# Performance work log

Hardware: AMD Instinct MI355X
Metric: run time of the kernel (lower is better)

Reference implementation:

```python
import jax, jax.numpy as jnp
import numpy as np

B, T, N_DYN, D_H, D_Z, HID = 256, 1024, 20, 64, 128, 64


def setup_inputs() -> dict:
    key = jax.random.key(0)
    ks = jax.random.split(key, 12)

    def uinit(k, shape):
        lim = 1.0 / np.sqrt(shape[0])
        return jax.random.uniform(k, shape, jnp.float32, -lim, lim)

    return dict(
        z0=jax.random.normal(ks[0], (B, D_Z), jnp.float32),
        # non-decreasing event times per sample (hours)
        t_dyn=jnp.cumsum(jax.random.uniform(ks[1], (B, T), jnp.float32), axis=1),
        Y_dyn=jax.random.normal(ks[2], (B, T, N_DYN), jnp.float32),
        M_dyn=jax.random.uniform(ks[3], (B, T, N_DYN), jnp.float32),
        H_dyn=jax.random.normal(ks[4], (B, T, D_H), jnp.float32),  # h_path.query(t_k) per step
        dyn_lens=jax.random.randint(ks[5], (B,), 0, T),
        ode_W0=uinit(ks[6], (D_Z, HID)), ode_b0=jnp.zeros((HID,), jnp.float32),
        ode_W1=uinit(ks[7], (HID, HID)), ode_b1=jnp.zeros((HID,), jnp.float32),
        ode_W2=uinit(ks[8], (HID, D_Z)), ode_b2=jnp.zeros((D_Z,), jnp.float32),
        W_ih=uinit(ks[9], (2 * N_DYN + D_H, 3 * D_Z)), b_ih=jnp.zeros((3 * D_Z,), jnp.float32),
        W_hh=uinit(ks[10], (D_Z, 3 * D_Z)), b_hh=jnp.zeros((3 * D_Z,), jnp.float32),
    )


def reference(z0, t_dyn, Y_dyn, M_dyn, H_dyn, dyn_lens,
              ode_W0, ode_b0, ode_W1, ode_b1, ode_W2, ode_b2,
              W_ih, b_ih, W_hh, b_hh):
    def ode_f(z):
        h = jnp.tanh(z @ ode_W0 + ode_b0)
        h = jnp.tanh(h @ ode_W1 + ode_b1)
        return h @ ode_W2 + ode_b2

    def evolve(z, dt):  # dt: (B,1); single-step RK4 of dz/ds = f(z)*dt over s in [0,1]
        f = lambda z_: ode_f(z_) * dt
        k1 = f(z)
        k2 = f(z + 0.5 * k1)
        k3 = f(z + 0.5 * k2)
        k4 = f(z + k3)
        return z + (k1 + 2.0 * k2 + 2.0 * k3 + k4) / 6.0

    def gru(x, h):  # torch GRUCell math
        gi = x @ W_ih + b_ih
        gh = h @ W_hh + b_hh
        i_r, i_u, i_n = jnp.split(gi, 3, axis=-1)
        h_r, h_u, h_n = jnp.split(gh, 3, axis=-1)
        r = jax.nn.sigmoid(i_r + h_r)
        u = jax.nn.sigmoid(i_u + h_u)
        n = jnp.tanh(i_n + r * h_n)
        return (1.0 - u) * n + u * h

    def step(carry, xs):
        z, t_prev = carry
        t_k, y_k, m_k, h_k, k = xs
        dt = jnp.clip(t_k - t_prev, 0.0)[:, None]
        # at k==0 dt is exactly 0 so evolve(z,0)==z, matching the torch k==0 branch
        z_ode = evolve(z, dt)
        inp = jnp.concatenate([y_k, m_k, h_k], axis=-1)  # (B, 2*n_dyn + d_h)
        z_new = gru(inp, z_ode)
        active = (k < dyn_lens).astype(z.dtype)[:, None]
        z = z_new * active + z_ode * (1.0 - active)
        return (z, t_k), z

    Tm = t_dyn.shape[1]
    xs = (t_dyn.T,
          jnp.transpose(Y_dyn, (1, 0, 2)),
          jnp.transpose(M_dyn, (1, 0, 2)),
          jnp.transpose(H_dyn, (1, 0, 2)),
          jnp.arange(Tm))
    (z_final, _), Z = jax.lax.scan(step, (z0, t_dyn[:, 0]), xs)
    return z_final, jnp.transpose(Z, (1, 0, 2))  # (B,d_z), (B,T,d_z)
```

## Files before the change

### kernel.cpp

```cpp
#include <hip/hip_runtime.h>
#include <cstdint>
#include <cstddef>

#define B_    256
#define T_    1024
#define NDYN  20
#define DH    64
#define DZ    128
#define HIDN  64
#define GCOLS 384
#define XDIM  104

#define WHH_LDS_G 25
#define WHH_REG   28

__device__ __forceinline__ int cpad(int k) { return (k >> 4) * 20 + (k & 15); }

template<int CTRL, int XORMASK>
__device__ __forceinline__ float dpp_sum(float v) {
#if __has_builtin(__builtin_amdgcn_mov_dpp)
  int o = __builtin_amdgcn_mov_dpp(__float_as_int(v), CTRL, 0xF, 0xF, true);
  return v + __int_as_float(o);
#else
  return v + __shfl_xor(v, XORMASK);
#endif
}

__device__ __forceinline__ float tanh_fast(float x) {
  float a = __expf(-2.f * fabsf(x));
  return copysignf((1.f - a) / (1.f + a), x);
}
__device__ __forceinline__ float sigm(float x) { return 1.f / (1.f + __expf(-x)); }

__global__ __launch_bounds__(384, 1) void odernn_kernel(
    const float* __restrict__ z0, const float* __restrict__ tdyn,
    const float* __restrict__ Y, const float* __restrict__ Mm,
    const float* __restrict__ Hh, const int* __restrict__ lens,
    const float* __restrict__ W0, const float* __restrict__ b0,
    const float* __restrict__ W1, const float* __restrict__ b1,
    const float* __restrict__ W2, const float* __restrict__ b2,
    const float* __restrict__ Wih, const float* __restrict__ bih,
    const float* __restrict__ Whh, const float* __restrict__ bhh,
    const float* __restrict__ gi_pre, float* __restrict__ out, int use_gi)
{
  const int tid = threadIdx.x;
  const int b   = blockIdx.x;

  __shared__ __align__(16) float vinP[160];
  __shared__ __align__(16) float h1P[80];
  __shared__ __align__(16) float h2P[80];
  __shared__ __align__(16) float zodeL[128];
  __shared__ float zcurL[128];
  __shared__ float gateL[384];
  __shared__ float gateN[128];
  __shared__ float xsL[112];
  __shared__ __align__(16) float4 WhhP4[WHH_LDS_G * 384];

  float wA[32], wB[32], whh28[WHH_REG];

  #pragma unroll 1
  for (int g = 0; g < WHH_LDS_G; ++g) {
    float4 w;
    w.x = Whh[(4 * g + 0) * GCOLS + tid];
    w.y = Whh[(4 * g + 1) * GCOLS + tid];
    w.z = Whh[(4 * g + 2) * GCOLS + tid];
    w.w = Whh[(4 * g + 3) * GCOLS + tid];
    WhhP4[g * 384 + tid] = w;
  }
  #pragma unroll
  for (int i = 0; i < WHH_REG; ++i)
    whh28[i] = Whh[(4 * WHH_LDS_G + i) * GCOLS + tid];

  if (tid < 256) {
    const int jg = tid >> 3, p = tid & 7, j0 = 2 * jg, kb = 16 * p;
    #pragma unroll
    for (int i = 0; i < 16; ++i) {
      wA[i]      = W0[(kb + i) * HIDN + j0];
      wA[16 + i] = W0[(kb + i) * HIDN + j0 + 1];
    }
  } else {
    const int u = tid - 128, jg = u >> 2, p = u & 3, j0 = 2 * jg, kb = 16 * p;
    #pragma unroll
    for (int i = 0; i < 16; ++i) {
      wA[i]      = W2[(kb + i) * DZ + j0];
      wA[16 + i] = W2[(kb + i) * DZ + j0 + 1];
    }
  }
  if (tid < 128) {
    const int jg = tid >> 2, p = tid & 3, j0 = 2 * jg, kb = 16 * p;
    #pragma unroll
    for (int i = 0; i < 16; ++i) {
      wB[i]      = W1[(kb + i) * HIDN + j0];
      wB[16 + i] = W1[(kb + i) * HIDN + j0 + 1];
    }
  } else if (tid < 256) {
    const int u = tid - 128, jg = u >> 2, p = u & 3, j0 = 2 * jg, kb = 16 * p;
    #pragma unroll
    for (int i = 0; i < 16; ++i) {
      wB[i]      = W2[(kb + i) * DZ + j0];
      wB[16 + i] = W2[(kb + i) * DZ + j0 + 1];
    }
  }

  float b0r = 0.f, b1r = 0.f, b2r = 0.f;
  if (tid < 256 && (tid & 7) < 2) b0r = b0[2 * (tid >> 3) + (tid & 7)];
  if (tid < 128 && (tid & 3) < 2) b1r = b1[2 * (tid >> 2) + (tid & 3)];
  if (tid >= 128 && ((tid - 128) & 3) < 2)
    b2r = b2[2 * ((tid - 128) >> 2) + ((tid - 128) & 3)];
  const float bhhr = bhh[tid];
  const float bihr = bih[tid];
  const int   lenb = lens[b];

  if (tid < 128) {
    float zv = z0[(size_t)b * DZ + tid];
    vinP[cpad(tid)] = zv;
    zcurL[tid] = zv;
  }
  __syncthreads();

  float* Zbase = out + (size_t)B_ * DZ;
  const float* tdb = tdyn + (size_t)b * T_;

  const int u2 = tid - 128, jg2 = u2 >> 2, p2 = u2 & 3;
  const int j2 = 2 * jg2 + p2;

  #pragma unroll 1
  for (int t = 0; t < T_; ++t) {
    const size_t bt = (size_t)b * T_ + t;
    const float dt = (t == 0) ? 0.f : fmaxf(tdb[t] - tdb[t - 1], 0.f);

    float gival = 0.f;
    if (use_gi) {
      gival = gi_pre[bt * GCOLS + tid];
    } else if (tid < XDIM) {
      float v;
      if (tid < 20)      v = Y[bt * NDYN + tid];
      else if (tid < 40) v = Mm[bt * NDYN + (tid - 20)];
      else               v = Hh[bt * DH + (tid - 40)];
      xsL[tid] = v;
    }

    float zreg = 0.f, kacc = 0.f;
    if (tid >= 128 && p2 < 2) zreg = zcurL[j2];

    #pragma unroll 1
    for (int e = 0; e < 4; ++e) {
      if (tid < 256) {
        const int p = tid & 7, jg = tid >> 3;
        const float4* vp = (const float4*)&vinP[p * 20];
        float a0 = 0.f, a1 = 0.f;
        #pragma unroll
        for (int q = 0; q < 4; ++q) {
          float4 v = vp[q];
          a0 += wA[4*q+0]*v.x + wA[4*q+1]*v.y + wA[4*q+2]*v.z + wA[4*q+3]*v.w;
          a1 += wA[16+4*q+0]*v.x + wA[16+4*q+1]*v.y + wA[16+4*q+2]*v.z + wA[16+4*q+3]*v.w;
        }
        a0 = dpp_sum<0xB1,1>(a0); a0 = dpp_sum<0x4E,2>(a0); a0 = dpp_sum<0x141,4>(a0);
        a1 = dpp_sum<0xB1,1>(a1); a1 = dpp_sum<0x4E,2>(a1); a1 = dpp_sum<0x141,4>(a1);
        if (p < 2)
          h1P[cpad(2 * jg + p)] = tanh_fast((p ? a1 : a0) + b0r);
      }
      __syncthreads();
      if (tid < 128) {
        const int p = tid & 3, jg = tid >> 2;
        const float4* hp = (const float4*)&h1P[p * 20];
        float a0 = 0.f, a1 = 0.f;
        #pragma unroll
        for (int q = 0; q < 4; ++q) {
          float4 v = hp[q];
          a0 += wB[4*q+0]*v.x + wB[4*q+1]*v.y + wB[4*q+2]*v.z + wB[4*q+3]*v.w;
          a1 += wB[16+4*q+0]*v.x + wB[16+4*q+1]*v.y + wB[16+4*q+2]*v.z + wB[16+4*q+3]*v.w;
        }
        a0 = dpp_sum<0xB1,1>(a0); a0 = dpp_sum<0x4E,2>(a0);
        a1 = dpp_sum<0xB1,1>(a1); a1 = dpp_sum<0x4E,2>(a1);
        if (p < 2)
          h2P[cpad(2 * jg + p)] = tanh_fast((p ? a1 : a0) + b1r);
      }
      __syncthreads();
      if (tid >= 128) {
        const float4* hp = (const float4*)&h2P[p2 * 20];
        float a0 = 0.f, a1 = 0.f;
        if (tid < 256) {
          #pragma unroll
          for (int q = 0; q < 4; ++q) {
            float4 v = hp[q];
            a0 += wB[4*q+0]*v.x + wB[4*q+1]*v.y + wB[4*q+2]*v.z + wB[4*q+3]*v.w;
            a1 += wB[16+4*q+0]*v.x + wB[16+4*q+1]*v.y + wB[16+4*q+2]*v.z + wB[16+4*q+3]*v.w;
          }
        } else {
          #pragma unroll
          for (int q = 0; q < 4; ++q) {
            float4 v = hp[q];
            a0 += wA[4*q+0]*v.x + wA[4*q+1]*v.y + wA[4*q+2]*v.z + wA[4*q+3]*v.w;
            a1 += wA[16+4*q+0]*v.x + wA[16+4*q+1]*v.y + wA[16+4*q+2]*v.z + wA[16+4*q+3]*v.w;
          }
        }
        a0 = dpp_sum<0xB1,1>(a0); a0 = dpp_sum<0x4E,2>(a0);
        a1 = dpp_sum<0xB1,1>(a1); a1 = dpp_sum<0x4E,2>(a1);
        if (p2 < 2) {
          const float kv = dt * ((p2 ? a1 : a0) + b2r);
          if (e == 0)      kacc = kv;
          else if (e == 3) kacc += kv;
          else             kacc += 2.f * kv;
          if (e < 3) {
            const float a = (e == 2) ? 1.f : 0.5f;
            vinP[cpad(j2)] = zreg + a * kv;
          } else {
            zodeL[j2] = zreg + kacc * (1.f / 6.f);
          }
        }
      }
      __syncthreads();
    }

    {
      float gh0 = bhhr, gh1 = 0.f;
      const float4* zq = (const float4*)zodeL;
      #pragma unroll 1
      for (int g = 0; g < WHH_LDS_G - 1; g += 2) {
        float4 w0 = WhhP4[g * 384 + tid];
        float4 w1 = WhhP4[(g + 1) * 384 + tid];
        float4 za = zq[g];
        float4 zb = zq[g + 1];
        gh0 += w0.x*za.x + w0.y*za.y + w0.z*za.z + w0.w*za.w;
        gh1 += w1.x*zb.x + w1.y*zb.y + w1.z*zb.z + w1.w*zb.w;
      }
      {
        float4 w0 = WhhP4[(WHH_LDS_G - 1) * 384 + tid];
        float4 za = zq[WHH_LDS_G - 1];
        gh0 += w0.x*za.x + w0.y*za.y + w0.z*za.z + w0.w*za.w;
      }
      #pragma unroll
      for (int q = 0; q < 7; ++q) {
        float4 z = zq[WHH_LDS_G + q];
        gh1 += whh28[4*q+0]*z.x + whh28[4*q+1]*z.y + whh28[4*q+2]*z.z + whh28[4*q+3]*z.w;
      }
      float gh = gh0 + gh1;
      float gi;
      if (use_gi) gi = gival;
      else {
        gi = bihr;
        for (int i = 0; i < XDIM; ++i) gi += xsL[i] * Wih[(size_t)i * GCOLS + tid];
      }
      if (tid < 256) gateL[tid] = gi + gh;
      else { gateL[tid] = gh; gateN[tid - 256] = gi; }
    }
    __syncthreads();

    if (tid < 128) {
      const float r  = sigm(gateL[tid]);
      const float uu = sigm(gateL[128 + tid]);
      const float n  = tanh_fast(gateN[tid] + r * gateL[256 + tid]);
      const float zo = zodeL[tid];
      const float zn = (1.f - uu) * n + uu * zo;
      const float znew = (t < lenb) ? zn : zo;
      vinP[cpad(tid)] = znew;
      zcurL[tid] = znew;
      Zbase[bt * DZ + tid] = znew;
    }
    __syncthreads();
  }

  if (tid < 128) out[(size_t)b * DZ + tid] = zcurL[tid];
}

__global__ __launch_bounds__(384) void gi_precompute(
    const float* __restrict__ Y, const float* __restrict__ Mm,
    const float* __restrict__ Hh, const float* __restrict__ Wih,
    const float* __restrict__ bih, float* __restrict__ gi)
{
  __shared__ float Xs[XDIM][16];
  const int tid = threadIdx.x;
  const size_t bt0 = (size_t)blockIdx.x * 16;
  for (int idx = tid; idx < XDIM * 16; idx += 384) {
    int r = idx & 15, c = idx >> 4;
    size_t bt = bt0 + r;
    float v;
    if (c < 20)      v = Y[bt * NDYN + c];
    else if (c < 40) v = Mm[bt * NDYN + (c - 20)];
    else             v = Hh[bt * DH + (c - 40)];
    Xs[c][r] = v;
  }
  __syncthreads();
  float acc[16];
  const float bv = bih[tid];
  #pragma unroll
  for (int r = 0; r < 16; ++r) acc[r] = bv;
  for (int i = 0; i < XDIM; ++i) {
    float w = Wih[i * GCOLS + tid];
    const float4* xp = (const float4*)(&Xs[i][0]);
    #pragma unroll
    for (int q = 0; q < 4; ++q) {
      float4 xv = xp[q];
      acc[4*q + 0] += xv.x * w;
      acc[4*q + 1] += xv.y * w;
      acc[4*q + 2] += xv.z * w;
      acc[4*q + 3] += xv.w * w;
    }
  }
  #pragma unroll
  for (int r = 0; r < 16; ++r) gi[(bt0 + r) * GCOLS + tid] = acc[r];
}

extern "C" void kernel_launch(void* const* d_in, const int* in_sizes, int n_in,
                              void* d_out, int out_size, void* d_ws, size_t ws_size,
                              hipStream_t stream) {
  const float* z0   = (const float*)d_in[0];
  const float* tdyn = (const float*)d_in[1];
  const float* Y    = (const float*)d_in[2];
  const float* Mm   = (const float*)d_in[3];
  const float* Hh   = (const float*)d_in[4];
  const int*   lens = (const int*)d_in[5];
  const float* W0   = (const float*)d_in[6];
  const float* b0   = (const float*)d_in[7];
  const float* W1   = (const float*)d_in[8];
  const float* b1   = (const float*)d_in[9];
  const float* W2   = (const float*)d_in[10];
  const float* b2   = (const float*)d_in[11];
  const float* Wih  = (const float*)d_in[12];
  const float* bih  = (const float*)d_in[13];
  const float* Whh  = (const float*)d_in[14];
  const float* bhh  = (const float*)d_in[15];
  float* out = (float*)d_out;

  const size_t gi_bytes = (size_t)B_ * T_ * GCOLS * sizeof(float);
  const int use_gi = (ws_size >= gi_bytes) ? 1 : 0;
  float* gi = (float*)d_ws;

  if (use_gi)
    gi_precompute<<<(B_ * T_) / 16, 384, 0, stream>>>(Y, Mm, Hh, Wih, bih, gi);

  odernn_kernel<<<B_, 384, 0, stream>>>(
      z0, tdyn, Y, Mm, Hh, lens, W0, b0, W1, b1, W2, b2,
      Wih, bih, Whh, bhh, use_gi ? gi : nullptr, out, use_gi);
}
```

Before: 5.247 ms.

## Widen ODE MLP stages to 512 threads, one output per thread group

Raises the block size from 384 to 512 threads and remaps the three ODE MLP matvecs so every thread takes part and each thread group produces a single output column instead of two. This shortens the per-thread dot products on the serial RK4 critical path. It also replaces __syncthreads with a raw LDS waitcnt plus s_barrier to trim barrier overhead. The cost is an extra wave per block that sits idle during the GRU gate stage, and possible register pressure at 512 threads.

New measurement: 5.029 ms. 4.2% less time.

```diff
diff --git a/kernel.cpp b/kernel.cpp
--- a/kernel.cpp
+++ b/kernel.cpp
@@ -10,11 +10,15 @@
 #define HIDN  64
 #define GCOLS 384
 #define XDIM  104
+#define THR   512
 
 #define WHH_LDS_G 25
 #define WHH_REG   28
 
 __device__ __forceinline__ int cpad(int k) { return (k >> 4) * 20 + (k & 15); }
+
+#define BAR() do { asm volatile("s_waitcnt lgkmcnt(0)" ::: "memory"); \
+                   __builtin_amdgcn_s_barrier(); } while (0)
 
 template<int CTRL, int XORMASK>
 __device__ __forceinline__ float dpp_sum(float v) {
@@ -32,7 +36,7 @@
 }
 __device__ __forceinline__ float sigm(float x) { return 1.f / (1.f + __expf(-x)); }
 
-__global__ __launch_bounds__(384, 1) void odernn_kernel(
+__global__ __launch_bounds__(THR, 1) void odernn_kernel(
     const float* __restrict__ z0, const float* __restrict__ tdyn,
     const float* __restrict__ Y, const float* __restrict__ Mm,
     const float* __restrict__ Hh, const int* __restrict__ lens,
@@ -56,59 +60,39 @@
   __shared__ float xsL[112];
   __shared__ __align__(16) float4 WhhP4[WHH_LDS_G * 384];
 
-  float wA[32], wB[32], whh28[WHH_REG];
-
-  #pragma unroll 1
-  for (int g = 0; g < WHH_LDS_G; ++g) {
-    float4 w;
-    w.x = Whh[(4 * g + 0) * GCOLS + tid];
-    w.y = Whh[(4 * g + 1) * GCOLS + tid];
-    w.z = Whh[(4 * g + 2) * GCOLS + tid];
-    w.w = Whh[(4 * g + 3) * GCOLS + tid];
-    WhhP4[g * 384 + tid] = w;
+  const int jg0 = tid >> 3, p0 = tid & 7;
+  const int j2  = tid >> 2, p2 = tid & 3;
+  const int gcol = (tid < GCOLS) ? tid : 0;
+
+  float w0r[16], w1r[8], w2r[16], whh28[WHH_REG];
+
+  if (tid < GCOLS) {
+    #pragma unroll 1
+    for (int g = 0; g < WHH_LDS_G; ++g) {
+      float4 w;
+      w.x = Whh[(4 * g + 0) * GCOLS + tid];
+      w.y = Whh[(4 * g + 1) * GCOLS + tid];
+      w.z = Whh[(4 * g + 2) * GCOLS + tid];
+      w.w = Whh[(4 * g + 3) * GCOLS + tid];
+      WhhP4[g * 384 + tid] = w;
+    }
   }
   #pragma unroll
   for (int i = 0; i < WHH_REG; ++i)
-    whh28[i] = Whh[(4 * WHH_LDS_G + i) * GCOLS + tid];
-
-  if (tid < 256) {
-    const int jg = tid >> 3, p = tid & 7, j0 = 2 * jg, kb = 16 * p;
-    #pragma unroll
-    for (int i = 0; i < 16; ++i) {
-      wA[i]      = W0[(kb + i) * HIDN + j0];
-      wA[16 + i] = W0[(kb + i) * HIDN + j0 + 1];
-    }
-  } else {
-    const int u = tid - 128, jg = u >> 2, p = u & 3, j0 = 2 * jg, kb = 16 * p;
-    #pragma unroll
-    for (int i = 0; i < 16; ++i) {
-      wA[i]      = W2[(kb + i) * DZ + j0];
-      wA[16 + i] = W2[(kb + i) * DZ + j0 + 1];
-    }
-  }
-  if (tid < 128) {
-    const int jg = tid >> 2, p = tid & 3, j0 = 2 * jg, kb = 16 * p;
-    #pragma unroll
-    for (int i = 0; i < 16; ++i) {
-      wB[i]      = W1[(kb + i) * HIDN + j0];
-      wB[16 + i] = W1[(kb + i) * HIDN + j0 + 1];
-    }
-  } else if (tid < 256) {
-    const int u = tid - 128, jg = u >> 2, p = u & 3, j0 = 2 * jg, kb = 16 * p;
-    #pragma unroll
-    for (int i = 0; i < 16; ++i) {
-      wB[i]      = W2[(kb + i) * DZ + j0];
-      wB[16 + i] = W2[(kb + i) * DZ + j0 + 1];
-    }
-  }
+    whh28[i] = Whh[(4 * WHH_LDS_G + i) * GCOLS + gcol];
+
+  #pragma unroll
+  for (int i = 0; i < 16; ++i) w0r[i] = W0[(16 * p0 + i) * HIDN + jg0];
+  #pragma unroll
+  for (int i = 0; i < 8; ++i)  w1r[i] = W1[(8 * p0 + i) * HIDN + jg0];
+  #pragma unroll
+  for (int i = 0; i < 16; ++i) w2r[i] = W2[(16 * p2 + i) * DZ + j2];
 
   float b0r = 0.f, b1r = 0.f, b2r = 0.f;
-  if (tid < 256 && (tid & 7) < 2) b0r = b0[2 * (tid >> 3) + (tid & 7)];
-  if (tid < 128 && (tid & 3) < 2) b1r = b1[2 * (tid >> 2) + (tid & 3)];
-  if (tid >= 128 && ((tid - 128) & 3) < 2)
-    b2r = b2[2 * ((tid - 128) >> 2) + ((tid - 128) & 3)];
-  const float bhhr = bhh[tid];
-  const float bihr = bih[tid];
+  if (p0 == 0) { b0r = b0[jg0]; b1r = b1[jg0]; }
+  if (p2 == 0) b2r = b2[j2];
+  const float bhhr = bhh[gcol];
+  const float bihr = bih[gcol];
   const int   lenb = lens[b];
 
   if (tid < 128) {
@@ -121,9 +105,6 @@
   float* Zbase = out + (size_t)B_ * DZ;
   const float* tdb = tdyn + (size_t)b * T_;
 
-  const int u2 = tid - 128, jg2 = u2 >> 2, p2 = u2 & 3;
-  const int j2 = 2 * jg2 + p2;
-
   #pragma unroll 1
   for (int t = 0; t < T_; ++t) {
     const size_t bt = (size_t)b * T_ + t;
@@ -131,7 +112,7 @@
 
     float gival = 0.f;
     if (use_gi) {
-      gival = gi_pre[bt * GCOLS + tid];
+      if (tid < GCOLS) gival = gi_pre[bt * GCOLS + tid];
     } else if (tid < XDIM) {
       float v;
       if (tid < 20)      v = Y[bt * NDYN + tid];
@@ -141,64 +122,44 @@
     }
 
     float zreg = 0.f, kacc = 0.f;
-    if (tid >= 128 && p2 < 2) zreg = zcurL[j2];
+    if (p2 == 0) zreg = zcurL[j2];
 
     #pragma unroll 1
     for (int e = 0; e < 4; ++e) {
-      if (tid < 256) {
-        const int p = tid & 7, jg = tid >> 3;
-        const float4* vp = (const float4*)&vinP[p * 20];
-        float a0 = 0.f, a1 = 0.f;
+      {
+        const float4* vp = (const float4*)&vinP[p0 * 20];
+        float a0 = 0.f;
         #pragma unroll
         for (int q = 0; q < 4; ++q) {
           float4 v = vp[q];
-          a0 += wA[4*q+0]*v.x + wA[4*q+1]*v.y + wA[4*q+2]*v.z + wA[4*q+3]*v.w;
-          a1 += wA[16+4*q+0]*v.x + wA[16+4*q+1]*v.y + wA[16+4*q+2]*v.z + wA[16+4*q+3]*v.w;
+          a0 += w0r[4*q+0]*v.x + w0r[4*q+1]*v.y + w0r[4*q+2]*v.z + w0r[4*q+3]*v.w;
         }
         a0 = dpp_sum<0xB1,1>(a0); a0 = dpp_sum<0x4E,2>(a0); a0 = dpp_sum<0x141,4>(a0);
-        a1 = dpp_sum<0xB1,1>(a1); a1 = dpp_sum<0x4E,2>(a1); a1 = dpp_sum<0x141,4>(a1);
-        if (p < 2)
-          h1P[cpad(2 * jg + p)] = tanh_fast((p ? a1 : a0) + b0r);
-      }
-      __syncthreads();
-      if (tid < 128) {
-        const int p = tid & 3, jg = tid >> 2;
-        const float4* hp = (const float4*)&h1P[p * 20];
-        float a0 = 0.f, a1 = 0.f;
+        if (p0 == 0)
+          h1P[cpad(jg0)] = tanh_fast(a0 + b0r);
+      }
+      BAR();
+      {
+        const float4* hp = (const float4*)&h1P[cpad(8 * p0)];
+        float4 v0 = hp[0], v1 = hp[1];
+        float a0 = w1r[0]*v0.x + w1r[1]*v0.y + w1r[2]*v0.z + w1r[3]*v0.w
+                 + w1r[4]*v1.x + w1r[5]*v1.y + w1r[6]*v1.z + w1r[7]*v1.w;
+        a0 = dpp_sum<0xB1,1>(a0); a0 = dpp_sum<0x4E,2>(a0); a0 = dpp_sum<0x141,4>(a0);
+        if (p0 == 0)
+          h2P[cpad(jg0)] = tanh_fast(a0 + b1r);
+      }
+      BAR();
+      {
+        const float4* hp = (const float4*)&h2P[p2 * 20];
+        float a0 = 0.f;
         #pragma unroll
         for (int q = 0; q < 4; ++q) {
           float4 v = hp[q];
-          a0 += wB[4*q+0]*v.x + wB[4*q+1]*v.y + wB[4*q+2]*v.z + wB[4*q+3]*v.w;
-          a1 += wB[16+4*q+0]*v.x + wB[16+4*q+1]*v.y + wB[16+4*q+2]*v.z + wB[16+4*q+3]*v.w;
+          a0 += w2r[4*q+0]*v.x + w2r[4*q+1]*v.y + w2r[4*q+2]*v.z + w2r[4*q+3]*v.w;
         }
         a0 = dpp_sum<0xB1,1>(a0); a0 = dpp_sum<0x4E,2>(a0);
-        a1 = dpp_sum<0xB1,1>(a1); a1 = dpp_sum<0x4E,2>(a1);
-        if (p < 2)
-          h2P[cpad(2 * jg + p)] = tanh_fast((p ? a1 : a0) + b1r);
-      }
-      __syncthreads();
-      if (tid >= 128) {
-        const float4* hp = (const float4*)&h2P[p2 * 20];
-        float a0 = 0.f, a1 = 0.f;
-        if (tid < 256) {
-          #pragma unroll
-          for (int q = 0; q < 4; ++q) {
-            float4 v = hp[q];
-            a0 += wB[4*q+0]*v.x + wB[4*q+1]*v.y + wB[4*q+2]*v.z + wB[4*q+3]*v.w;
-            a1 += wB[16+4*q+0]*v.x + wB[16+4*q+1]*v.y + wB[16+4*q+2]*v.z + wB[16+4*q+3]*v.w;
-          }
-        } else {
-          #pragma unroll
-          for (int q = 0; q < 4; ++q) {
-            float4 v = hp[q];
-            a0 += wA[4*q+0]*v.x + wA[4*q+1]*v.y + wA[4*q+2]*v.z + wA[4*q+3]*v.w;
-            a1 += wA[16+4*q+0]*v.x + wA[16+4*q+1]*v.y + wA[16+4*q+2]*v.z + wA[16+4*q+3]*v.w;
-          }
-        }
-        a0 = dpp_sum<0xB1,1>(a0); a0 = dpp_sum<0x4E,2>(a0);
-        a1 = dpp_sum<0xB1,1>(a1); a1 = dpp_sum<0x4E,2>(a1);
-        if (p2 < 2) {
-          const float kv = dt * ((p2 ? a1 : a0) + b2r);
+        if (p2 == 0) {
+          const float kv = dt * (a0 + b2r);
           if (e == 0)      kacc = kv;
           else if (e == 3) kacc += kv;
           else             kacc += 2.f * kv;
@@ -210,10 +171,10 @@
           }
         }
       }
-      __syncthreads();
-    }
-
-    {
+      BAR();
+    }
+
+    if (tid < GCOLS) {
       float gh0 = bhhr, gh1 = 0.f;
       const float4* zq = (const float4*)zodeL;
       #pragma unroll 1
@@ -245,7 +206,7 @@
       if (tid < 256) gateL[tid] = gi + gh;
       else { gateL[tid] = gh; gateN[tid - 256] = gi; }
     }
-    __syncthreads();
+    BAR();
 
     if (tid < 128) {
       const float r  = sigm(gateL[tid]);
@@ -258,9 +219,10 @@
       zcurL[tid] = znew;
       Zbase[bt * DZ + tid] = znew;
     }
-    __syncthreads();
-  }
-
+    BAR();
+  }
+
+  __syncthreads();
   if (tid < 128) out[(size_t)b * DZ + tid] = zcurL[tid];
 }
 
@@ -330,7 +292,7 @@
   if (use_gi)
     gi_precompute<<<(B_ * T_) / 16, 384, 0, stream>>>(Y, Mm, Hh, Wih, bih, gi);
 
-  odernn_kernel<<<B_, 384, 0, stream>>>(
+  odernn_kernel<<<B_, THR, 0, stream>>>(
       z0, tdyn, Y, Mm, Hh, lens, W0, b0, W1, b1, W2, b2,
       Wih, bih, Whh, bhh, use_gi ? gi : nullptr, out, use_gi);
 }
```
